# Performance work log

Hardware: AMD Instinct MI355X
Metric: run time of the kernel (lower is better)

## Reference

```python
import jax, jax.numpy as jnp
import numpy as np

IN_FEATURES = 256
OUT_FEATURES = 64
ALPHA = 0.2  # leaky relu slope


def _xavier_uniform(key, shape, gain=1.414):
    fan_in, fan_out = shape[0], shape[1]
    limit = gain * np.sqrt(6.0 / (fan_in + fan_out))
    return jax.random.uniform(key, shape, jnp.float32, -limit, limit)


def setup_inputs() -> dict:
    key = jax.random.key(0)
    k_h, k_W, k_a = jax.random.split(key, 3)
    h = jax.random.normal(k_h, (8, 2048, IN_FEATURES), dtype=jnp.float32)
    W = _xavier_uniform(k_W, (IN_FEATURES, OUT_FEATURES))
    a = _xavier_uniform(k_a, (2 * OUT_FEATURES, 1))
    return {"h": h, "W": W, "a": a}


def reference(h, W, a):
    # h: [B, N, F_in], W: [F_in, D], a: [2D, 1]
    Wh = h @ W  # [B, N, D]
    D = Wh.shape[-1]
    a1 = a[:D, 0]   # attends to source node i (repeat_interleave side)
    a2 = a[D:, 0]   # attends to target node j (repeat side)
    f1 = Wh @ a1    # [B, N]
    f2 = Wh @ a2    # [B, N]
    # e[b, i, j] = leakyrelu(a1.Wh[b,i] + a2.Wh[b,j])  -- identical math to
    # the original's O(N^2 * 2D) repeat/concat, without materializing it.
    e = jax.nn.leaky_relu(f1[:, :, None] + f2[:, None, :], negative_slope=ALPHA)  # [B, N, N]
    # NOTE: original applies softmax over dim=1 (over i, per column j).
    attention = jax.nn.softmax(e, axis=1)  # [B, N, N]
    # dropout is identity in eval mode
    h_prime = jnp.einsum('bij,bjd->bid', attention, Wh)  # [B, N, D]
    return jax.nn.elu(h_prime)  # concat=True path
```

## Files before the change

kernel.cpp:

```cpp
#include <hip/hip_runtime.h>

#define B 8
#define N 2048
#define KF 256
#define DF 64
#define LOG2E 1.44269504088896340736f
#define IC 8
#define ICH (N / IC)

typedef __attribute__((ext_vector_type(8))) short short8;
typedef __attribute__((ext_vector_type(4))) float float4v;

__device__ __forceinline__ float fexp2(float x) {
#if __has_builtin(__builtin_amdgcn_exp2f)
    return __builtin_amdgcn_exp2f(x);
#else
    return exp2f(x);
#endif
}
__device__ __forceinline__ float flog2(float x) {
#if __has_builtin(__builtin_amdgcn_logf)
    return __builtin_amdgcn_logf(x);
#else
    return log2f(x);
#endif
}
__device__ __forceinline__ float eluf(float x) {
    return x > 0.f ? x : fexp2(x * LOG2E) - 1.0f;
}
__device__ __forceinline__ short bf16r(float x) {
    unsigned u = __float_as_uint(x);
    return (short)((u + 0x8000u) >> 16);
}
#define DOT4(c, u, p) \
    p = fmaf(c.x, u.x, fmaf(c.y, u.y, fmaf(c.z, u.z, fmaf(c.w, u.w, p))));

__global__ __launch_bounds__(256) void k_wh(const float* __restrict__ h,
                                            const float* __restrict__ W,
                                            const float* __restrict__ a,
                                            short* __restrict__ WhT,
                                            float* __restrict__ f1,
                                            float* __restrict__ f2) {
    __shared__ __align__(16) unsigned char smem[34816];
    short* lwt  = (short*)smem;
    float* lv   = (float*)(smem + 32768);
    float* lred = (float*)smem;
    float* lp   = (float*)(smem + 16896);

    int t = threadIdx.x;
    int wv = t >> 6, lane = t & 63;
    int n15 = lane & 15, q = lane >> 4;
    int bx = blockIdx.x;

    const float* hr = h + ((long)bx * 32 + n15) * KF + wv * 64 + q * 8;
    float4 c0 = *(const float4*)(hr);
    float4 c1 = *(const float4*)(hr + 4);
    float4 c2 = *(const float4*)(hr + 32);
    float4 c3 = *(const float4*)(hr + 36);

    {
        const float4* wr4 = (const float4*)(W + t * DF);
        float s1 = 0.f, s2 = 0.f;
        #pragma unroll
        for (int c = 0; c < 16; c++) {
            float4 w4 = wr4[c];
            float4 a1v = *(const float4*)(a + 4 * c);
            float4 a2v = *(const float4*)(a + DF + 4 * c);
            lwt[(4 * c + 0) * 256 + t] = bf16r(w4.x);
            lwt[(4 * c + 1) * 256 + t] = bf16r(w4.y);
            lwt[(4 * c + 2) * 256 + t] = bf16r(w4.z);
            lwt[(4 * c + 3) * 256 + t] = bf16r(w4.w);
            s1 = fmaf(w4.x, a1v.x, fmaf(w4.y, a1v.y, fmaf(w4.z, a1v.z, fmaf(w4.w, a1v.w, s1))));
            s2 = fmaf(w4.x, a2v.x, fmaf(w4.y, a2v.y, fmaf(w4.z, a2v.z, fmaf(w4.w, a2v.w, s2))));
        }
        lv[t] = s1;
        lv[256 + t] = s2;
    }
    __syncthreads();

    const short* bq = lwt + n15 * 256 + wv * 64 + q * 8;
    short8 s0b0 = *(const short8*)(bq);
    short8 s0b1 = *(const short8*)(bq + 16 * 256);
    short8 s0b2 = *(const short8*)(bq + 32 * 256);
    short8 s0b3 = *(const short8*)(bq + 48 * 256);
    short8 s1b0 = *(const short8*)(bq + 32);
    short8 s1b1 = *(const short8*)(bq + 16 * 256 + 32);
    short8 s1b2 = *(const short8*)(bq + 32 * 256 + 32);
    short8 s1b3 = *(const short8*)(bq + 48 * 256 + 32);
    const float* vv = lv + wv * 64 + q * 8;
    float4 u00 = *(const float4*)(vv);
    float4 u01 = *(const float4*)(vv + 4);
    float4 u10 = *(const float4*)(vv + 32);
    float4 u11 = *(const float4*)(vv + 36);
    float4 x00 = *(const float4*)(vv + 256);
    float4 x01 = *(const float4*)(vv + 256 + 4);
    float4 x10 = *(const float4*)(vv + 256 + 32);
    float4 x11 = *(const float4*)(vv + 256 + 36);
    __syncthreads();

    #pragma unroll
    for (int rt = 0; rt < 2; rt++) {
        float4 m0, m1, m2, m3;
        if (rt < 1) {
            const float* hn = hr + 16 * KF;
            m0 = *(const float4*)(hn);
            m1 = *(const float4*)(hn + 4);
            m2 = *(const float4*)(hn + 32);
            m3 = *(const float4*)(hn + 36);
        }
        float p1 = 0.f, p2 = 0.f;
        DOT4(c0, u00, p1) DOT4(c1, u01, p1) DOT4(c2, u10, p1) DOT4(c3, u11, p1)
        DOT4(c0, x00, p2) DOT4(c1, x01, p2) DOT4(c2, x10, p2) DOT4(c3, x11, p2)

        short8 af0 = { bf16r(c0.x), bf16r(c0.y), bf16r(c0.z), bf16r(c0.w),
                       bf16r(c1.x), bf16r(c1.y), bf16r(c1.z), bf16r(c1.w) };
        short8 af1 = { bf16r(c2.x), bf16r(c2.y), bf16r(c2.z), bf16r(c2.w),
                       bf16r(c3.x), bf16r(c3.y), bf16r(c3.z), bf16r(c3.w) };
        float4v acc0 = {0.f, 0.f, 0.f, 0.f}, acc1 = acc0, acc2 = acc0, acc3 = acc0;
        acc0 = __builtin_amdgcn_mfma_f32_16x16x32_bf16(af0, s0b0, acc0, 0, 0, 0);
        acc0 = __builtin_amdgcn_mfma_f32_16x16x32_bf16(af1, s1b0, acc0, 0, 0, 0);
        acc1 = __builtin_amdgcn_mfma_f32_16x16x32_bf16(af0, s0b1, acc1, 0, 0, 0);
        acc1 = __builtin_amdgcn_mfma_f32_16x16x32_bf16(af1, s1b1, acc1, 0, 0, 0);
        acc2 = __builtin_amdgcn_mfma_f32_16x16x32_bf16(af0, s0b2, acc2, 0, 0, 0);
        acc2 = __builtin_amdgcn_mfma_f32_16x16x32_bf16(af1, s1b2, acc2, 0, 0, 0);
        acc3 = __builtin_amdgcn_mfma_f32_16x16x32_bf16(af0, s0b3, acc3, 0, 0, 0);
        acc3 = __builtin_amdgcn_mfma_f32_16x16x32_bf16(af1, s1b3, acc3, 0, 0, 0);

        #define STASH(nb, A)                                                  \
            {                                                                 \
                _Pragma("unroll")                                             \
                for (int r = 0; r < 4; r++)                                   \
                    lred[wv * 1056 + (q * 4 + r) * 66 + nb * 16 + n15] = A[r]; \
            }
        STASH(0, acc0) STASH(1, acc1) STASH(2, acc2) STASH(3, acc3)
        #undef STASH
        p1 += __shfl_xor(p1, 16, 64); p1 += __shfl_xor(p1, 32, 64);
        p2 += __shfl_xor(p2, 16, 64); p2 += __shfl_xor(p2, 32, 64);
        if (q == 0) { lp[wv * 16 + n15] = p1; lp[64 + wv * 16 + n15] = p2; }
        __syncthreads();

        long i0 = (long)bx * 32 + rt * 16;
        int d = t & 63, ig = t >> 6;
        int bb = (int)(i0 >> 11);
        int il = (int)(i0 & (N - 1));
        float s0 = 0.f, s1 = 0.f, s2 = 0.f, s3 = 0.f;
        #pragma unroll
        for (int w = 0; w < 4; w++) {
            const float* lr = lred + w * 1056 + (ig * 4) * 66 + d;
            s0 += lr[0]; s1 += lr[66]; s2 += lr[132]; s3 += lr[198];
        }
        short4 pk = make_short4(bf16r(s0), bf16r(s1), bf16r(s2), bf16r(s3));
        int jj = il + ig * 4;
        *(short4*)(WhT + (((long)bb * 16 + (jj >> 7)) * 64 + d) * 128 + (jj & 127)) = pk;

        if (t < 16) {
            f1[i0 + t] = lp[t] + lp[16 + t] + lp[32 + t] + lp[48 + t];
        } else if (t < 32) {
            int tt = t + 48;
            f2[i0 + t - 16] = lp[tt] + lp[16 + tt] + lp[32 + tt] + lp[48 + tt];
        }
        __syncthreads();
        c0 = m0; c1 = m1; c2 = m2; c3 = m3;
    }
}

__global__ __launch_bounds__(256) void k_denom(const float* __restrict__ f1,
                                               const float* __restrict__ f2,
                                               float* __restrict__ dpart) {
    __shared__ float lf1[ICH];
    int t = threadIdx.x;
    int b = blockIdx.z, ic = blockIdx.y;
    int j = blockIdx.x * 256 + t;
    lf1[t] = f1[b * N + ic * ICH + t];
    __syncthreads();
    float f2j = f2[b * N + j] * LOG2E;
    float s = 0.f;
    const float4* lf4 = (const float4*)lf1;
    for (int ii = 0; ii < ICH / 4; ii++) {
        float4 v = lf4[ii];
        float e0 = fmaf(v.x, LOG2E, f2j);
        float e1 = fmaf(v.y, LOG2E, f2j);
        float e2 = fmaf(v.z, LOG2E, f2j);
        float e3 = fmaf(v.w, LOG2E, f2j);
        s += fexp2(fmaxf(e0, 0.2f * e0));
        s += fexp2(fmaxf(e1, 0.2f * e1));
        s += fexp2(fmaxf(e2, 0.2f * e2));
        s += fexp2(fmaxf(e3, 0.2f * e3));
    }
    dpart[((long)ic * B + b) * N + j] = s;
}

__global__ __launch_bounds__(512) void k_attn(const short* __restrict__ WhT,
                                              const float* __restrict__ f1,
                                              const float* __restrict__ f2,
                                              const float* __restrict__ dpart,
                                              float* __restrict__ out) {
    __shared__ uint4 ls[2][64 * 17];
    __shared__ float2 lc[2][2][128];
    int t = threadIdx.x;
    int wv = t >> 6, lane = t & 63;
    int g = wv >> 2, wg = wv & 3, lt = t & 255;
    int n15 = lane & 15, q = lane >> 4;
    int it = blockIdx.x, b = blockIdx.y;
    int i0 = it * 64 + wg * 16;

    float f1L = f1[b * N + i0 + n15] * LOG2E;
    const uint4* wsrc = (const uint4*)WhT + ((long)b * 16 + g * 8) * 1024;
    const float* f2b = f2 + b * N + g * 1024;
    const float* dpb = dpart + b * N + g * 1024;

    uint4 r0, r1, r2, r3;
    float pf2, pd0, pd1, pd2, pd3, pd4, pd5, pd6, pd7;

    #define LOADC(cc) {                                     \
        const uint4* gp = wsrc + (cc) * 1024;               \
        r0 = gp[lt];       r1 = gp[256 + lt];               \
        r2 = gp[512 + lt]; r3 = gp[768 + lt];               \
    }
    #define LOADP(cc) {                                     \
        if (lt < 128) {                                     \
            int jb2 = (cc) * 128 + lt;                      \
            pf2 = f2b[jb2];                                 \
            pd0 = dpb[jb2];              pd1 = dpb[16384 + jb2]; \
            pd2 = dpb[2 * 16384 + jb2];  pd3 = dpb[3 * 16384 + jb2]; \
            pd4 = dpb[4 * 16384 + jb2];  pd5 = dpb[5 * 16384 + jb2]; \
            pd6 = dpb[6 * 16384 + jb2];  pd7 = dpb[7 * 16384 + jb2]; \
        }                                                   \
    }
    #define STOREC() {                                      \
        int rb = lt >> 4, cl = lt & 15;                     \
        ls[g][rb * 17 + cl] = r0;                           \
        ls[g][(16 + rb) * 17 + cl] = r1;                    \
        ls[g][(32 + rb) * 17 + cl] = r2;                    \
        ls[g][(48 + rb) * 17 + cl] = r3;                    \
    }
    #define LCC(buf) {                                      \
        if (lt < 128) {                                     \
            float den = ((pd0 + pd1) + (pd2 + pd3)) + ((pd4 + pd5) + (pd6 + pd7)); \
            lc[g][buf][lt] = make_float2(pf2 * LOG2E, -flog2(den)); \
        }                                                   \
    }

    LOADC(0) LOADP(0)
    STOREC() LCC(0)
    __syncthreads();

    float4v acc0 = {0.f, 0.f, 0.f, 0.f}, acc1 = acc0, acc2 = acc0, acc3 = acc0;

    for (int c = 0; c < 8; c++) {
        int cur = c & 1;
        if (c < 7) { LOADC(c + 1) LOADP(c + 1) }

        const short* lsS = (const short*)&ls[g][0];
        const float4* lcf = (const float4*)&lc[g][cur][0];
        #pragma unroll
        for (int js = 0; js < 4; js++) {
            const float4* cp4 = lcf + js * 16 + q * 4;
            float4 p01 = cp4[0], p23 = cp4[1], p45 = cp4[2], p67 = cp4[3];
            short8 af;
            #define PENT(F2L, LS2, DI)                        \
                {                                             \
                    float t0 = f1L + (F2L);                   \
                    float l2 = fmaxf(t0, 0.2f * t0);          \
                    af[DI] = bf16r(fexp2(l2 + (LS2)));        \
                }
            PENT(p01.x, p01.y, 0) PENT(p01.z, p01.w, 1)
            PENT(p23.x, p23.y, 2) PENT(p23.z, p23.w, 3)
            PENT(p45.x, p45.y, 4) PENT(p45.z, p45.w, 5)
            PENT(p67.x, p67.y, 6) PENT(p67.z, p67.w, 7)
            #undef PENT

            const short* bp = lsS + js * 32 + q * 8;
            short8 b0 = *(const short8*)(bp + (n15 +  0) * 136);
            short8 b1 = *(const short8*)(bp + (n15 + 16) * 136);
            short8 b2 = *(const short8*)(bp + (n15 + 32) * 136);
            short8 b3 = *(const short8*)(bp + (n15 + 48) * 136);

            acc0 = __builtin_amdgcn_mfma_f32_16x16x32_bf16(af, b0, acc0, 0, 0, 0);
            acc1 = __builtin_amdgcn_mfma_f32_16x16x32_bf16(af, b1, acc1, 0, 0, 0);
            acc2 = __builtin_amdgcn_mfma_f32_16x16x32_bf16(af, b2, acc2, 0, 0, 0);
            acc3 = __builtin_amdgcn_mfma_f32_16x16x32_bf16(af, b3, acc3, 0, 0, 0);
        }

        if (c < 7) {
            __syncthreads();
            STOREC() LCC((c + 1) & 1)
            __syncthreads();
        }
    }
    #undef LOADC
    #undef LOADP
    #undef STOREC
    #undef LCC

    __syncthreads();
    float* epi = (float*)&ls[0][0];
    #define ESTASH(nb, A)                                                    \
        {                                                                    \
            _Pragma("unroll")                                                \
            for (int r = 0; r < 4; r++)                                      \
                epi[g * 4224 + (wg * 16 + q * 4 + r) * 66 + nb * 16 + n15] = A[r]; \
        }
    ESTASH(0, acc0) ESTASH(1, acc1) ESTASH(2, acc2) ESTASH(3, acc3)
    #undef ESTASH
    __syncthreads();

    int row = t >> 3, d0 = (t & 7) * 8;
    const float* e0p = epi + row * 66 + d0;
    const float* e1p = epi + 4224 + row * 66 + d0;
    float4 a0 = *(const float4*)(e0p);
    float4 a1 = *(const float4*)(e0p + 4);
    float4 b0 = *(const float4*)(e1p);
    float4 b1 = *(const float4*)(e1p + 4);
    float4 o0, o1;
    o0.x = eluf(a0.x + b0.x); o0.y = eluf(a0.y + b0.y);
    o0.z = eluf(a0.z + b0.z); o0.w = eluf(a0.w + b0.w);
    o1.x = eluf(a1.x + b1.x); o1.y = eluf(a1.y + b1.y);
    o1.z = eluf(a1.z + b1.z); o1.w = eluf(a1.w + b1.w);
    float* op = out + ((long)b * N + it * 64 + row) * DF + d0;
    *(float4*)(op) = o0;
    *(float4*)(op + 4) = o1;
}

extern "C" void kernel_launch(void* const* d_in, const int* in_sizes, int n_in,
                              void* d_out, int out_size, void* d_ws, size_t ws_size,
                              hipStream_t stream) {
    const float* h = (const float*)d_in[0];
    const float* W = (const float*)d_in[1];
    const float* a = (const float*)d_in[2];
    float* out = (float*)d_out;

    char* ws = (char*)d_ws;
    const size_t NB = (size_t)B * N;
    size_t off = 0;
    short* WhT   = (short*)(ws + off); off += NB * DF * sizeof(short);
    float* f1    = (float*)(ws + off); off += NB * sizeof(float);
    float* f2    = (float*)(ws + off); off += NB * sizeof(float);
    float* dpart = (float*)(ws + off); off += (size_t)IC * NB * sizeof(float);
    (void)off; (void)ws_size;

    k_wh<<<NB / 32, 256, 0, stream>>>(h, W, a, WhT, f1, f2);
    k_denom<<<dim3(N / 256, IC, B), 256, 0, stream>>>(f1, f2, dpart);
    k_attn<<<dim3(N / 64, B), 512, 0, stream>>>(WhT, f1, f2, dpart, out);
}
```

Before: 97.82 us.

## Factor leaky-relu exponentials into separable products and split j across four wave groups

The exponential of leakyrelu(f1+f2) is rewritten as max(exp(f1)exp(f2), exp(0.2f1)exp(0.2f2)), so the per-element exp in both the denominator and attention kernels becomes multiplies and a max on precomputed per-row and per-column factors. The softmax denominator is folded in as a reciprocal multiplier rather than a log offset. The attention kernel now gives each wave 32 rows and splits the j dimension across four groups with 64-wide chunks, and the WhT layout is retiled to match. A two-phase shared-memory epilogue reduces the four partial sums. Risk: exp(f) may overflow or lose precision without max-subtraction if f values are large, and more accumulators raise register pressure.

```diff
diff --git a/kernel.cpp b/kernel.cpp
--- a/kernel.cpp
+++ b/kernel.cpp
@@ -16,13 +16,6 @@
     return __builtin_amdgcn_exp2f(x);
 #else
     return exp2f(x);
-#endif
-}
-__device__ __forceinline__ float flog2(float x) {
-#if __has_builtin(__builtin_amdgcn_logf)
-    return __builtin_amdgcn_logf(x);
-#else
-    return log2f(x);
 #endif
 }
 __device__ __forceinline__ float eluf(float x) {
@@ -151,7 +144,7 @@
         }
         short4 pk = make_short4(bf16r(s0), bf16r(s1), bf16r(s2), bf16r(s3));
         int jj = il + ig * 4;
-        *(short4*)(WhT + (((long)bb * 16 + (jj >> 7)) * 64 + d) * 128 + (jj & 127)) = pk;
+        *(short4*)(WhT + (((long)bb * 32 + (jj >> 6)) * 64 + d) * 64 + (jj & 63)) = pk;
 
         if (t < 16) {
             f1[i0 + t] = lp[t] + lp[16 + t] + lp[32 + t] + lp[48 + t];
@@ -167,25 +160,22 @@
 __global__ __launch_bounds__(256) void k_denom(const float* __restrict__ f1,
                                                const float* __restrict__ f2,
                                                float* __restrict__ dpart) {
-    __shared__ float lf1[ICH];
+    __shared__ float2 le[ICH];
     int t = threadIdx.x;
     int b = blockIdx.z, ic = blockIdx.y;
     int j = blockIdx.x * 256 + t;
-    lf1[t] = f1[b * N + ic * ICH + t];
-    __syncthreads();
-    float f2j = f2[b * N + j] * LOG2E;
+    float v = f1[b * N + ic * ICH + t];
+    le[t] = make_float2(fexp2(v * LOG2E), fexp2(v * 0.2f * LOG2E));
+    __syncthreads();
+    float f2j = f2[b * N + j];
+    float E2  = fexp2(f2j * LOG2E);
+    float E2s = fexp2(f2j * 0.2f * LOG2E);
     float s = 0.f;
-    const float4* lf4 = (const float4*)lf1;
-    for (int ii = 0; ii < ICH / 4; ii++) {
-        float4 v = lf4[ii];
-        float e0 = fmaf(v.x, LOG2E, f2j);
-        float e1 = fmaf(v.y, LOG2E, f2j);
-        float e2 = fmaf(v.z, LOG2E, f2j);
-        float e3 = fmaf(v.w, LOG2E, f2j);
-        s += fexp2(fmaxf(e0, 0.2f * e0));
-        s += fexp2(fmaxf(e1, 0.2f * e1));
-        s += fexp2(fmaxf(e2, 0.2f * e2));
-        s += fexp2(fmaxf(e3, 0.2f * e3));
+    const float4* le4 = (const float4*)le;
+    for (int ii = 0; ii < ICH / 2; ii++) {
+        float4 u = le4[ii];
+        s += fmaxf(u.x * E2, u.y * E2s);
+        s += fmaxf(u.z * E2, u.w * E2s);
     }
     dpart[((long)ic * B + b) * N + j] = s;
 }
@@ -195,31 +185,36 @@
                                               const float* __restrict__ f2,
                                               const float* __restrict__ dpart,
                                               float* __restrict__ out) {
-    __shared__ uint4 ls[2][64 * 17];
-    __shared__ float2 lc[2][2][128];
+    __shared__ __align__(16) unsigned char smem[40960];
     int t = threadIdx.x;
     int wv = t >> 6, lane = t & 63;
-    int g = wv >> 2, wg = wv & 3, lt = t & 255;
+    int g = wv >> 1, wg = wv & 1, lt2 = t & 127;
     int n15 = lane & 15, q = lane >> 4;
     int it = blockIdx.x, b = blockIdx.y;
-    int i0 = it * 64 + wg * 16;
-
-    float f1L = f1[b * N + i0 + n15] * LOG2E;
-    const uint4* wsrc = (const uint4*)WhT + ((long)b * 16 + g * 8) * 1024;
-    const float* f2b = f2 + b * N + g * 1024;
-    const float* dpb = dpart + b * N + g * 1024;
+    int i0 = it * 64 + wg * 32;
+
+    float f1a = f1[b * N + i0 + n15];
+    float f1b = f1[b * N + i0 + 16 + n15];
+    float E1a = fexp2(f1a * LOG2E),  E1sa = fexp2(f1a * 0.2f * LOG2E);
+    float E1b = fexp2(f1b * LOG2E),  E1sb = fexp2(f1b * 0.2f * LOG2E);
+
+    uint4*  ls = (uint4*)smem + g * 576;
+    float2* lc = (float2*)(smem + 36864) + g * 128;
+    const uint4* wsrc = (const uint4*)WhT + ((long)b * 32 + g * 8) * 512;
+    const float* f2b = f2 + b * N + g * 512;
+    const float* dpb = dpart + b * N + g * 512;
 
     uint4 r0, r1, r2, r3;
     float pf2, pd0, pd1, pd2, pd3, pd4, pd5, pd6, pd7;
 
     #define LOADC(cc) {                                     \
-        const uint4* gp = wsrc + (cc) * 1024;               \
-        r0 = gp[lt];       r1 = gp[256 + lt];               \
-        r2 = gp[512 + lt]; r3 = gp[768 + lt];               \
+        const uint4* gp = wsrc + (cc) * 512;                \
+        r0 = gp[lt2];       r1 = gp[128 + lt2];             \
+        r2 = gp[256 + lt2]; r3 = gp[384 + lt2];             \
     }
     #define LOADP(cc) {                                     \
-        if (lt < 128) {                                     \
-            int jb2 = (cc) * 128 + lt;                      \
+        if (lt2 < 64) {                                     \
+            int jb2 = (cc) * 64 + lt2;                      \
             pf2 = f2b[jb2];                                 \
             pd0 = dpb[jb2];              pd1 = dpb[16384 + jb2]; \
             pd2 = dpb[2 * 16384 + jb2];  pd3 = dpb[3 * 16384 + jb2]; \
@@ -228,16 +223,17 @@
         }                                                   \
     }
     #define STOREC() {                                      \
-        int rb = lt >> 4, cl = lt & 15;                     \
-        ls[g][rb * 17 + cl] = r0;                           \
-        ls[g][(16 + rb) * 17 + cl] = r1;                    \
-        ls[g][(32 + rb) * 17 + cl] = r2;                    \
-        ls[g][(48 + rb) * 17 + cl] = r3;                    \
+        int rb = lt2 >> 3, cl = lt2 & 7;                    \
+        ls[rb * 9 + cl] = r0;        ls[(16 + rb) * 9 + cl] = r1; \
+        ls[(32 + rb) * 9 + cl] = r2; ls[(48 + rb) * 9 + cl] = r3; \
     }
     #define LCC(buf) {                                      \
-        if (lt < 128) {                                     \
+        if (lt2 < 64) {                                     \
             float den = ((pd0 + pd1) + (pd2 + pd3)) + ((pd4 + pd5) + (pd6 + pd7)); \
-            lc[g][buf][lt] = make_float2(pf2 * LOG2E, -flog2(den)); \
+            float rr = 1.0f / den;                          \
+            float E2  = fexp2(pf2 * LOG2E);                 \
+            float E2s = fexp2(pf2 * 0.2f * LOG2E);          \
+            lc[(buf) * 64 + lt2] = make_float2(E2 * rr, E2s * rr); \
         }                                                   \
     }
 
@@ -245,41 +241,44 @@
     STOREC() LCC(0)
     __syncthreads();
 
-    float4v acc0 = {0.f, 0.f, 0.f, 0.f}, acc1 = acc0, acc2 = acc0, acc3 = acc0;
+    float4v accA0 = {0.f, 0.f, 0.f, 0.f}, accA1 = accA0, accA2 = accA0, accA3 = accA0;
+    float4v accB0 = accA0, accB1 = accA0, accB2 = accA0, accB3 = accA0;
 
     for (int c = 0; c < 8; c++) {
         int cur = c & 1;
         if (c < 7) { LOADC(c + 1) LOADP(c + 1) }
 
-        const short* lsS = (const short*)&ls[g][0];
-        const float4* lcf = (const float4*)&lc[g][cur][0];
+        const short* lsS = (const short*)ls;
+        const float4* lcf = (const float4*)(lc + cur * 64);
         #pragma unroll
-        for (int js = 0; js < 4; js++) {
+        for (int js = 0; js < 2; js++) {
             const float4* cp4 = lcf + js * 16 + q * 4;
             float4 p01 = cp4[0], p23 = cp4[1], p45 = cp4[2], p67 = cp4[3];
-            short8 af;
-            #define PENT(F2L, LS2, DI)                        \
-                {                                             \
-                    float t0 = f1L + (F2L);                   \
-                    float l2 = fmaxf(t0, 0.2f * t0);          \
-                    af[DI] = bf16r(fexp2(l2 + (LS2)));        \
-                }
-            PENT(p01.x, p01.y, 0) PENT(p01.z, p01.w, 1)
-            PENT(p23.x, p23.y, 2) PENT(p23.z, p23.w, 3)
-            PENT(p45.x, p45.y, 4) PENT(p45.z, p45.w, 5)
-            PENT(p67.x, p67.y, 6) PENT(p67.z, p67.w, 7)
-            #undef PENT
+            short8 afA, afB;
+            #define PE(px, py, DI) {                                  \
+                afA[DI] = bf16r(fmaxf(E1a * (px), E1sa * (py)));      \
+                afB[DI] = bf16r(fmaxf(E1b * (px), E1sb * (py)));      \
+            }
+            PE(p01.x, p01.y, 0) PE(p01.z, p01.w, 1)
+            PE(p23.x, p23.y, 2) PE(p23.z, p23.w, 3)
+            PE(p45.x, p45.y, 4) PE(p45.z, p45.w, 5)
+            PE(p67.x, p67.y, 6) PE(p67.z, p67.w, 7)
+            #undef PE
 
             const short* bp = lsS + js * 32 + q * 8;
-            short8 b0 = *(const short8*)(bp + (n15 +  0) * 136);
-            short8 b1 = *(const short8*)(bp + (n15 + 16) * 136);
-            short8 b2 = *(const short8*)(bp + (n15 + 32) * 136);
-            short8 b3 = *(const short8*)(bp + (n15 + 48) * 136);
-
-            acc0 = __builtin_amdgcn_mfma_f32_16x16x32_bf16(af, b0, acc0, 0, 0, 0);
-            acc1 = __builtin_amdgcn_mfma_f32_16x16x32_bf16(af, b1, acc1, 0, 0, 0);
-            acc2 = __builtin_amdgcn_mfma_f32_16x16x32_bf16(af, b2, acc2, 0, 0, 0);
-            acc3 = __builtin_amdgcn_mfma_f32_16x16x32_bf16(af, b3, acc3, 0, 0, 0);
+            short8 b0 = *(const short8*)(bp + (n15 +  0) * 72);
+            short8 b1 = *(const short8*)(bp + (n15 + 16) * 72);
+            short8 b2 = *(const short8*)(bp + (n15 + 32) * 72);
+            short8 b3 = *(const short8*)(bp + (n15 + 48) * 72);
+
+            accA0 = __builtin_amdgcn_mfma_f32_16x16x32_bf16(afA, b0, accA0, 0, 0, 0);
+            accA1 = __builtin_amdgcn_mfma_f32_16x16x32_bf16(afA, b1, accA1, 0, 0, 0);
+            accA2 = __builtin_amdgcn_mfma_f32_16x16x32_bf16(afA, b2, accA2, 0, 0, 0);
+            accA3 = __builtin_amdgcn_mfma_f32_16x16x32_bf16(afA, b3, accA3, 0, 0, 0);
+            accB0 = __builtin_amdgcn_mfma_f32_16x16x32_bf16(afB, b0, accB0, 0, 0, 0);
+            accB1 = __builtin_amdgcn_mfma_f32_16x16x32_bf16(afB, b1, accB1, 0, 0, 0);
+            accB2 = __builtin_amdgcn_mfma_f32_16x16x32_bf16(afB, b2, accB2, 0, 0, 0);
+            accB3 = __builtin_amdgcn_mfma_f32_16x16x32_bf16(afB, b3, accB3, 0, 0, 0);
         }
 
         if (c < 7) {
@@ -293,31 +292,49 @@
     #undef STOREC
     #undef LCC
 
-    __syncthreads();
-    float* epi = (float*)&ls[0][0];
-    #define ESTASH(nb, A)                                                    \
-        {                                                                    \
-            _Pragma("unroll")                                                \
-            for (int r = 0; r < 4; r++)                                      \
-                epi[g * 4224 + (wg * 16 + q * 4 + r) * 66 + nb * 16 + n15] = A[r]; \
-        }
-    ESTASH(0, acc0) ESTASH(1, acc1) ESTASH(2, acc2) ESTASH(3, acc3)
+    float* epi = (float*)smem;
+    int row_o = t >> 3, d0 = (t & 7) * 8;
+    int wg_o = row_o >> 5, r31 = row_o & 31;
+    const float* e1p = epi + wg_o * 2176 + r31 * 68 + d0;
+    const float* e2p = epi + (2 + wg_o) * 2176 + r31 * 68 + d0;
+
+    #define ESTASH(rg) {                                                     \
+        float* ep = epi + (rg) * 2176 + (q * 4) * 68 + n15;                  \
+        _Pragma("unroll")                                                    \
+        for (int r = 0; r < 4; r++) {                                        \
+            ep[r * 68 +  0] = accA0[r]; ep[r * 68 + 16] = accA1[r];          \
+            ep[r * 68 + 32] = accA2[r]; ep[r * 68 + 48] = accA3[r];          \
+            ep[(16 * 68) + r * 68 +  0] = accB0[r];                          \
+            ep[(16 * 68) + r * 68 + 16] = accB1[r];                          \
+            ep[(16 * 68) + r * 68 + 32] = accB2[r];                          \
+            ep[(16 * 68) + r * 68 + 48] = accB3[r];                          \
+        }                                                                    \
+    }
+
+    __syncthreads();
+    if (g < 2) ESTASH(wv)
+    __syncthreads();
+    float4 sa0 = *(const float4*)(e1p);
+    float4 sa1 = *(const float4*)(e1p + 4);
+    float4 sb0 = *(const float4*)(e2p);
+    float4 sb1 = *(const float4*)(e2p + 4);
+    float4 t0, t1;
+    t0.x = sa0.x + sb0.x; t0.y = sa0.y + sb0.y; t0.z = sa0.z + sb0.z; t0.w = sa0.w + sb0.w;
+    t1.x = sa1.x + sb1.x; t1.y = sa1.y + sb1.y; t1.z = sa1.z + sb1.z; t1.w = sa1.w + sb1.w;
+    __syncthreads();
+    if (g >= 2) ESTASH(wv - 4)
+    __syncthreads();
     #undef ESTASH
-    __syncthreads();
-
-    int row = t >> 3, d0 = (t & 7) * 8;
-    const float* e0p = epi + row * 66 + d0;
-    const float* e1p = epi + 4224 + row * 66 + d0;
-    float4 a0 = *(const float4*)(e0p);
-    float4 a1 = *(const float4*)(e0p + 4);
-    float4 b0 = *(const float4*)(e1p);
-    float4 b1 = *(const float4*)(e1p + 4);
+    float4 ua0 = *(const float4*)(e1p);
+    float4 ua1 = *(const float4*)(e1p + 4);
+    float4 ub0 = *(const float4*)(e2p);
+    float4 ub1 = *(const float4*)(e2p + 4);
     float4 o0, o1;
-    o0.x = eluf(a0.x + b0.x); o0.y = eluf(a0.y + b0.y);
-    o0.z = eluf(a0.z + b0.z); o0.w = eluf(a0.w + b0.w);
-    o1.x = eluf(a1.x + b1.x); o1.y = eluf(a1.y + b1.y);
-    o1.z = eluf(a1.z + b1.z); o1.w = eluf(a1.w + b1.w);
-    float* op = out + ((long)b * N + it * 64 + row) * DF + d0;
+    o0.x = eluf(t0.x + ua0.x + ub0.x); o0.y = eluf(t0.y + ua0.y + ub0.y);
+    o0.z = eluf(t0.z + ua0.z + ub0.z); o0.w = eluf(t0.w + ua0.w + ub0.w);
+    o1.x = eluf(t1.x + ua1.x + ub1.x); o1.y = eluf(t1.y + ua1.y + ub1.y);
+    o1.z = eluf(t1.z + ua1.z + ub1.z); o1.w = eluf(t1.w + ua1.w + ub1.w);
+    float* op = out + ((long)b * N + it * 64 + row_o) * DF + d0;
     *(float4*)(op) = o0;
     *(float4*)(op + 4) = o1;
 }
```

Result: faster. 91.75 us (-6.2%).
